# Kernel optimization log

Hardware: AMD Instinct MI355X
Metric: run time of the kernel (lower is better)

The kernel has to match this reference:

```python
import jax, jax.numpy as jnp
import numpy as np

L, H, NH, HD, F, B, S = 32, 1024, 16, 64, 2048, 2, 2048
HPH = H // NH  # hidden per attention head (hyena column split)
EPS = 1e-6
BLOCK = {0:'HCS',4:'HCS',7:'HCS',11:'HCS',14:'HCS',18:'HCS',21:'HCS',25:'HCS',28:'HCS',
         1:'HCM',5:'HCM',8:'HCM',12:'HCM',15:'HCM',19:'HCM',22:'HCM',26:'HCM',29:'HCM',
         2:'HCL',6:'HCL',9:'HCL',13:'HCL',16:'HCL',20:'HCL',23:'HCL',27:'HCL',30:'HCL',
         3:'ATT',10:'ATT',17:'ATT',24:'ATT',31:'ATT'}

def rmsnorm(x, w):
    return x * jax.lax.rsqrt(jnp.mean(x * x, -1, keepdims=True) + EPS) * w

def step_fir(u, state, w, b, flip=False, gated=False):
    # u:[B,C]  state:[B,C,cache]  w:[C,Lf]  b:[C]  (single-token FIR step)
    cache = state.shape[-1]
    w = w[:, ::-1][:, -(cache + 1):] if flip else w[:, :cache + 1]
    y = w[:, -1] * u + jnp.sum(state * w[:, :-1], -1)
    y = y + (b * u if gated else b)
    return y

def split3(z):
    # column_split_hyena=True path of _interleave_split
    r = z.reshape(z.shape[0], NH, 3 * HPH)
    x2 = r[:, :, :HPH].reshape(z.shape[0], H)
    x1 = r[:, :, HPH:2 * HPH].reshape(z.shape[0], H)
    v = r[:, :, 2 * HPH:].reshape(z.shape[0], H)
    return x2, x1, v

def mlp(x, W1, W2):
    return jax.nn.gelu(x @ W1.T) @ W2.T

def fir_block(x, n1, n2, pW, pb, oW, ob, W1, W2, sfw, sfb, h, D, fstate, istate, flip, gated):
    xn = rmsnorm(x, n1)
    z = xn @ pW.T + pb                 # [B,1,3H]
    u = z[:, -1]                       # [B,3H]
    zp = step_fir(u, fstate, sfw, sfb)
    x2, x1, v = split3(zp)
    y = step_fir(x1 * v, istate, h, D, flip=flip, gated=gated)
    y = (y * x2)[:, None]              # [B,1,H]
    x = y @ oW.T + ob + x
    return mlp(rmsnorm(x, n2), W1, W2) + x

def hcl_block(x, n1, n2, pW, pb, oW, ob, W1, W2, sfw, sfb, log_poles, residues, D, fstate, iir):
    xn = rmsnorm(x, n1)
    z = xn @ pW.T + pb
    u = z[:, -1]
    zp = step_fir(u, fstate, sfw, sfb)
    x2, x1, v = split3(zp)
    x1v = x1 * v
    iir_new = jnp.exp(log_poles) * iir + x1v[..., None]   # [B,H,SS] single-step IIR update
    res = jnp.sum(residues * iir_new, -1)
    y = (x2 * (res + D * x1v))[:, None]
    x = y @ oW.T + ob + x
    return mlp(rmsnorm(x, n2), W1, W2) + x

def att_block(x, n1, n2, qW, qb, oW, ob, W1, W2, kc, vc, cos, sin, pos):
    xn = rmsnorm(x, n1)
    qkv = (xn @ qW.T + qb).reshape(B, 1, 3, NH, HD)
    q, k, v = qkv[:, :, 0], qkv[:, :, 1], qkv[:, :, 2]
    c = jnp.concatenate([cos[pos], cos[pos]])  # [HD]
    s = jnp.concatenate([sin[pos], sin[pos]])
    rot = lambda t: jnp.concatenate([-t[..., HD // 2:], t[..., :HD // 2]], -1)
    q = q * c + rot(q) * s
    k = k * c + rot(k) * s
    kc = kc.at[:, pos].set(k[:, 0])  # KV-cache scatter write at current position
    vc = vc.at[:, pos].set(v[:, 0])
    scores = jnp.einsum('bohd,bshd->bhos', q, kc) * (HD ** -0.5)
    scores = jnp.where(jnp.arange(S) > pos, -10000.0, scores)
    aw = jax.nn.softmax(scores, -1)
    ctx = jnp.einsum('bhos,bshd->bohd', aw, vc).reshape(B, 1, H)
    x = ctx @ oW.T + ob + x
    return mlp(rmsnorm(x, n2), W1, W2) + x

def forward(x, position, norm1_w, norm2_w, proj_W, proj_b, out_W, out_b, mlp_W1, mlp_W2,
            sf_w, sf_b, hcs_h, hcs_D, hcm_h, hcm_D, hcl_logpoles, hcl_residues, hcl_D,
            fir_state, hcs_state, hcm_state, iir_state, k_cache, v_cache, rope_cos, rope_sin):
    att = 0
    for i in range(L):  # loop over 32 structurally distinct layers (static)
        t = BLOCK[i]
        cm = (norm1_w[i], norm2_w[i], proj_W[i], proj_b[i], out_W[i], out_b[i], mlp_W1[i], mlp_W2[i])
        if t == 'HCS':
            x = fir_block(x, *cm, sf_w[i], sf_b[i], hcs_h[i], hcs_D[i], fir_state[i], hcs_state[i], False, False)
        elif t == 'HCM':
            x = fir_block(x, *cm, sf_w[i], sf_b[i], hcm_h[i], hcm_D[i], fir_state[i], hcm_state[i], True, True)
        elif t == 'HCL':
            x = hcl_block(x, *cm, sf_w[i], sf_b[i], hcl_logpoles[i], hcl_residues[i], hcl_D[i], fir_state[i], iir_state[i])
        else:
            x = att_block(x, *cm, k_cache[att], v_cache[att], rope_cos, rope_sin, position)
            att += 1
    return x

def setup_inputs():
    key = jax.random.key(0)
    ks = jax.random.split(key, 24)
    g = lambda k, shape, sc: jax.random.normal(k, shape, jnp.float32) * sc
    inv_freq = 1.0 / (10000.0 ** (np.arange(0, HD, 2, dtype=np.float32) / HD))
    ang = np.arange(S, dtype=np.float32)[:, None] * inv_freq[None, :]
    return {
        'x': g(ks[0], (B, 1, H), 1.0),
        'position': 1024,
        'norm1_w': jnp.ones((L, H), jnp.float32),
        'norm2_w': jnp.ones((L, H), jnp.float32),
        'proj_W': g(ks[1], (L, 3 * H, H), H ** -0.5),
        'proj_b': jnp.zeros((L, 3 * H), jnp.float32),
        'out_W': g(ks[2], (L, H, H), 0.2 * H ** -0.5),
        'out_b': jnp.zeros((L, H), jnp.float32),
        'mlp_W1': g(ks[3], (L, F, H), H ** -0.5),
        'mlp_W2': g(ks[4], (L, H, F), 0.2 * F ** -0.5),
        'sf_w': g(ks[5], (L, 3 * H, 3), 0.4),
        'sf_b': g(ks[6], (L, 3 * H), 0.02),
        'hcs_h': g(ks[7], (L, H, 7), 0.2),
        'hcs_D': g(ks[8], (L, H), 0.2),
        'hcm_h': g(ks[9], (L, H, 128), 0.04),
        'hcm_D': g(ks[10], (L, H), 0.2),
        'hcl_logpoles': -jax.random.uniform(ks[11], (L, H, 16), jnp.float32, 0.01, 2.0),
        'hcl_residues': g(ks[12], (L, H, 16), 0.1),
        'hcl_D': g(ks[13], (L, H), 0.2),
        'fir_state': g(ks[14], (L, B, 3 * H, 2), 0.5),
        'hcs_state': g(ks[15], (L, B, H, 6), 0.5),
        'hcm_state': g(ks[16], (L, B, H, 127), 0.5),
        'iir_state': g(ks[17], (L, B, H, 16), 0.5),
        'k_cache': g(ks[18], (5, B, S, NH, HD), 1.0),
        'v_cache': g(ks[19], (5, B, S, NH, HD), 1.0),
        'rope_cos': jnp.asarray(np.cos(ang)),
        'rope_sin': jnp.asarray(np.sin(ang)),
    }

def reference(x, position, norm1_w, norm2_w, proj_W, proj_b, out_W, out_b, mlp_W1, mlp_W2,
              sf_w, sf_b, hcs_h, hcs_D, hcm_h, hcm_D, hcl_logpoles, hcl_residues, hcl_D,
              fir_state, hcs_state, hcm_state, iir_state, k_cache, v_cache, rope_cos, rope_sin):
    return forward(x, position, norm1_w, norm2_w, proj_W, proj_b, out_W, out_b, mlp_W1, mlp_W2,
                   sf_w, sf_b, hcs_h, hcs_D, hcm_h, hcm_D, hcl_logpoles, hcl_residues, hcl_D,
                   fir_state, hcs_state, hcm_state, iir_state, k_cache, v_cache, rope_cos, rope_sin)
```

## Files before the change

### kernel.cpp

```cpp
#include <hip/hip_runtime.h>
#include <hip/hip_bf16.h>
#include <math.h>

#define LAYERS 32
#define H      1024
#define H3     3072
#define NHEADS 16
#define HDIM   64
#define FF     2048
#define BATCH  2
#define SEQ    2048
#define EPSF   1e-6f

__device__ __forceinline__ float wredSum(float v) {
#pragma unroll
  for (int m = 32; m >= 1; m >>= 1) v += __shfl_xor(v, m, 64);
  return v;
}
__device__ __forceinline__ float wredMax(float v) {
#pragma unroll
  for (int m = 32; m >= 1; m >>= 1) v = fmaxf(v, __shfl_xor(v, m, 64));
  return v;
}
__device__ __forceinline__ float gelu_t(float x) {
  return 0.5f * x * (1.0f + tanhf(0.7978845608028654f * (x + 0.044715f * x * x * x)));
}
__device__ __forceinline__ float dot4(float4 a, float4 b) {
  return a.x * b.x + a.y * b.y + a.z * b.z + a.w * b.w;
}

__global__ __launch_bounds__(256) void prep_kernel(
    const float* __restrict__ sf_w, const float* __restrict__ sf_b,
    const float* __restrict__ fir_state,
    const float* __restrict__ hcs_h, const float* __restrict__ hcs_D, const float* __restrict__ hcs_state,
    const float* __restrict__ hcm_h, const float* __restrict__ hcm_D, const float* __restrict__ hcm_state,
    const float* __restrict__ lp, const float* __restrict__ resd, const float* __restrict__ hcl_D,
    const float* __restrict__ iir,
    unsigned long long kbits,
    float* __restrict__ sfd, float* __restrict__ sfc,
    float* __restrict__ mix0, float* __restrict__ mix1)
{
  int blk = blockIdx.x, tid = threadIdx.x;
  if (blk < 768) {
    int idx = blk * 256 + tid;
    int i = idx / (BATCH * H3);
    int r = idx % (BATCH * H3);
    int b = r / H3, ch = r % H3;
    const float* fs = fir_state + ((size_t)(i * BATCH + b) * H3 + ch) * 2;
    const float* sw = sf_w + ((size_t)i * H3 + ch) * 3;
    sfd[idx] = fs[0] * sw[0] + fs[1] * sw[1] + sf_b[i * H3 + ch];
    if (b == 0) sfc[i * H3 + ch] = sw[2];
  } else if (blk < 1024) {
    int idx = (blk - 768) * 256 + tid;
    int i = idx >> 11;
    int r = idx & 2047;
    int b = r >> 10, c = r & 1023;
    int kind = (int)((kbits >> (2 * i)) & 3ull);
    if (kind == 0) {
      const float* st = hcs_state + ((size_t)(i * BATCH + b) * H + c) * 6;
      const float* hh = hcs_h + ((size_t)i * H + c) * 7;
      float acc = 0.f;
#pragma unroll
      for (int k = 0; k < 6; k++) acc += st[k] * hh[k];
      mix0[idx] = acc + hcs_D[i * H + c];
      if (b == 0) mix1[i * H + c] = hh[6];
    } else if (kind == 2) {
      const float* ii = iir + ((size_t)(i * BATCH + b) * H + c) * 16;
      const float* lpp = lp + ((size_t)i * H + c) * 16;
      const float* rs = resd + ((size_t)i * H + c) * 16;
      float acc = 0.f, rsum = 0.f;
#pragma unroll
      for (int k = 0; k < 16; k++) { float rv = rs[k]; acc += rv * expf(lpp[k]) * ii[k]; rsum += rv; }
      mix0[idx] = acc;
      if (b == 0) mix1[i * H + c] = rsum + hcl_D[i * H + c];
    }
  } else {
    int w = tid >> 6, lane = tid & 63;
    int widx = (blk - 1024) * 4 + w;
    if (widx < 9 * BATCH * H) {
      int li = widx >> 11;
      int r = widx & 2047;
      int b = r >> 10, c = r & 1023;
      int i = (li >> 1) * 7 + ((li & 1) ? 5 : 1);
      const float* st = hcm_state + ((size_t)(i * BATCH + b) * H + c) * 127;
      const float* hh = hcm_h + ((size_t)i * H + c) * 128;
      float acc = 0.f;
      int k = lane;
      if (k < 127) acc += st[k] * hh[127 - k];
      k = lane + 64;
      if (k < 127) acc += st[k] * hh[127 - k];
      acc = wredSum(acc);
      if (lane == 0) {
        mix0[(i * BATCH + b) * H + c] = acc;
        if (b == 0) mix1[i * H + c] = hh[0] + hcm_D[i * H + c];
      }
    }
  }
}

template<int ROWS, bool GELU, bool HASBIAS>
__global__ __launch_bounds__(256) void gemv_norm(
    const float* __restrict__ x, const float* __restrict__ nw,
    const float* __restrict__ W, const float* __restrict__ bias,
    float* __restrict__ out)
{
  __shared__ alignas(16) float xe[BATCH * H];
  __shared__ float red[8];
  int tid = threadIdx.x, lane = tid & 63, w = tid >> 6;

  float4 xv0 = ((const float4*)x)[tid];
  float4 xv1 = ((const float4*)x)[tid + 256];
  float4 nv  = ((const float4*)nw)[tid];
  int r = blockIdx.x * 4 + w;
  const float4* rowp = (const float4*)(W + (size_t)r * H);
  float4 wv0 = rowp[lane], wv1 = rowp[lane + 64],
         wv2 = rowp[lane + 128], wv3 = rowp[lane + 192];

  float ss0 = dot4(xv0, xv0), ss1 = dot4(xv1, xv1);
  ((float4*)xe)[tid]       = make_float4(xv0.x * nv.x, xv0.y * nv.y, xv0.z * nv.z, xv0.w * nv.w);
  ((float4*)xe)[tid + 256] = make_float4(xv1.x * nv.x, xv1.y * nv.y, xv1.z * nv.z, xv1.w * nv.w);
  ss0 = wredSum(ss0); ss1 = wredSum(ss1);
  if (lane == 0) { red[w] = ss0; red[4 + w] = ss1; }
  __syncthreads();
  float s0 = rsqrtf((red[0] + red[1] + red[2] + red[3]) * (1.0f / H) + EPSF);
  float s1 = rsqrtf((red[4] + red[5] + red[6] + red[7]) * (1.0f / H) + EPSF);

  const float4* x4 = (const float4*)xe;
  float a0 = dot4(wv0, x4[lane])       + dot4(wv1, x4[lane + 64])
           + dot4(wv2, x4[lane + 128]) + dot4(wv3, x4[lane + 192]);
  float a1 = dot4(wv0, x4[lane + 256]) + dot4(wv1, x4[lane + 320])
           + dot4(wv2, x4[lane + 384]) + dot4(wv3, x4[lane + 448]);
  a0 = wredSum(a0); a1 = wredSum(a1);
  if (lane == 0) {
    float b0 = HASBIAS ? bias[r] : 0.f;
    float v0 = a0 * s0 + b0, v1 = a1 * s1 + b0;
    if (GELU) { v0 = gelu_t(v0); v1 = gelu_t(v1); }
    out[r] = v0;
    out[ROWS + r] = v1;
  }
}

__global__ __launch_bounds__(256) void mix_out_kernel(
    int kind,
    const float* __restrict__ z, const float* __restrict__ sfdL, const float* __restrict__ sfcL,
    const float* __restrict__ mix0L, const float* __restrict__ mix1L,
    const float* __restrict__ attP,
    const float* __restrict__ oW, const float* __restrict__ ob,
    const float* __restrict__ x_in, float* __restrict__ x_out)
{
  __shared__ alignas(16) float ys[BATCH * H];
  int tid = threadIdx.x, lane = tid & 63, w = tid >> 6;
  int r = blockIdx.x * 4 + w;

  if (kind < 3) {
    float x2v[8], x1v[8], vvv[8];
#pragma unroll
    for (int it = 0; it < 8; it++) {
      int e = tid + it * 256;
      int b = e >> 10, c = e & 1023;
      int n = c >> 6, d = c & 63;
      int base = n * 192 + d;
      x2v[it] = sfcL[base] * z[b * H3 + base] + sfdL[b * H3 + base];
      x1v[it] = sfcL[base + 64] * z[b * H3 + base + 64] + sfdL[b * H3 + base + 64];
      vvv[it] = sfcL[base + 128] * z[b * H3 + base + 128] + sfdL[b * H3 + base + 128];
    }
    const float4* rowp = (const float4*)(oW + (size_t)r * H);
    float4 wv0 = rowp[lane], wv1 = rowp[lane + 64],
           wv2 = rowp[lane + 128], wv3 = rowp[lane + 192];
#pragma unroll
    for (int it = 0; it < 8; it++) {
      int e = tid + it * 256;
      int b = e >> 10, c = e & 1023;
      float t = x1v[it] * vvv[it];
      ys[e] = (mix1L[c] * t + mix0L[b * H + c]) * x2v[it];
    }
    __syncthreads();
    const float4* y4 = (const float4*)ys;
    float a0 = dot4(wv0, y4[lane])       + dot4(wv1, y4[lane + 64])
             + dot4(wv2, y4[lane + 128]) + dot4(wv3, y4[lane + 192]);
    float a1 = dot4(wv0, y4[lane + 256]) + dot4(wv1, y4[lane + 320])
             + dot4(wv2, y4[lane + 384]) + dot4(wv3, y4[lane + 448]);
    a0 = wredSum(a0); a1 = wredSum(a1);
    if (lane == 0) {
      x_out[r]     = a0 + ob[r] + x_in[r];
      x_out[H + r] = a1 + ob[r] + x_in[H + r];
    }
  } else {
    const float4* rowp = (const float4*)(oW + (size_t)r * H);
    float4 wv0 = rowp[lane], wv1 = rowp[lane + 64],
           wv2 = rowp[lane + 128], wv3 = rowp[lane + 192];
#pragma unroll
    for (int it = 0; it < 8; it++) {
      int e = tid + it * 256;
      int b = e >> 10, c = e & 1023;
      int n = c >> 6, d = c & 63;
      float M = -1e30f;
#pragma unroll
      for (int sp = 0; sp < 8; sp++) M = fmaxf(M, attP[((sp * BATCH + b) * NHEADS + n) * 66 + 64]);
      float Ls = 0.f, num = 0.f;
#pragma unroll
      for (int sp = 0; sp < 8; sp++) {
        const float* P = attP + ((sp * BATCH + b) * NHEADS + n) * 66;
        float wgt = expf(P[64] - M);
        Ls += wgt * P[65];
        num += wgt * P[d];
      }
      ys[e] = num / Ls;
    }
    __syncthreads();
    const float4* y4 = (const float4*)ys;
    float a0 = dot4(wv0, y4[lane])       + dot4(wv1, y4[lane + 64])
             + dot4(wv2, y4[lane + 128]) + dot4(wv3, y4[lane + 192]);
    float a1 = dot4(wv0, y4[lane + 256]) + dot4(wv1, y4[lane + 320])
             + dot4(wv2, y4[lane + 384]) + dot4(wv3, y4[lane + 448]);
    a0 = wredSum(a0); a1 = wredSum(a1);
    if (lane == 0) {
      x_out[r]     = a0 + ob[r] + x_in[r];
      x_out[H + r] = a1 + ob[r] + x_in[H + r];
    }
  }
}

__global__ __launch_bounds__(256) void gemv_mlp2(
    const float* __restrict__ h, const float* __restrict__ W2,
    const float* __restrict__ xM, float* __restrict__ x_out)
{
  __shared__ alignas(16) float hs[BATCH * FF];
  int tid = threadIdx.x, lane = tid & 63, w = tid >> 6;
  float4 h0 = ((const float4*)h)[tid];
  float4 h1 = ((const float4*)h)[tid + 256];
  float4 h2 = ((const float4*)h)[tid + 512];
  float4 h3 = ((const float4*)h)[tid + 768];
  int r = blockIdx.x * 4 + w;
  const float4* rowp = (const float4*)(W2 + (size_t)r * FF);
  float4 wv[8];
#pragma unroll
  for (int j = 0; j < 8; j++) wv[j] = rowp[lane + 64 * j];

  ((float4*)hs)[tid]       = h0;
  ((float4*)hs)[tid + 256] = h1;
  ((float4*)hs)[tid + 512] = h2;
  ((float4*)hs)[tid + 768] = h3;
  __syncthreads();

  const float4* h4 = (const float4*)hs;
  float a0 = 0.f, a1 = 0.f;
#pragma unroll
  for (int j = 0; j < 8; j++) {
    a0 += dot4(wv[j], h4[lane + 64 * j]);
    a1 += dot4(wv[j], h4[lane + 64 * j + 512]);
  }
  a0 = wredSum(a0); a1 = wredSum(a1);
  if (lane == 0) {
    x_out[r]     = a0 + xM[r];
    x_out[H + r] = a1 + xM[H + r];
  }
}

__global__ __launch_bounds__(256) void attn_kernel(
    const float* __restrict__ z, const int* __restrict__ posp,
    const float* __restrict__ kc, const float* __restrict__ vc,
    const float* __restrict__ cosT, const float* __restrict__ sinT,
    float* __restrict__ P)
{
  int sp = blockIdx.x & 7, n = (blockIdx.x >> 3) & 15, b = blockIdx.x >> 7;
  int pos = *posp;
  __shared__ alignas(16) float q_s[HDIM], k_s[HDIM], v_s[HDIM];
  __shared__ float eg[256];
  __shared__ float redA[4];
  __shared__ alignas(16) float osum[4][HDIM];
  int tid = threadIdx.x, lane = tid & 63, w = tid >> 6;

  if (tid < 64) {
    int d = tid, j = d & 31;
    float cs = cosT[pos * 32 + j], sn = sinT[pos * 32 + j];
    float qv = z[b * H3 + n * 64 + d];
    float qo = z[b * H3 + n * 64 + ((d + 32) & 63)];
    q_s[d] = ((d < 32) ? (qv * cs - qo * sn) : (qv * cs + qo * sn)) * 0.125f;
    float kv = z[b * H3 + 1024 + n * 64 + d];
    float ko = z[b * H3 + 1024 + n * 64 + ((d + 32) & 63)];
    k_s[d] = (d < 32) ? (kv * cs - ko * sn) : (kv * cs + ko * sn);
    v_s[d] = z[b * H3 + 2048 + n * 64 + d];
  }
  __syncthreads();

  int s = sp * 256 + tid;
  float logit = -1e30f;
  if (s <= pos) {
    const float4* k4 = (s == pos) ? (const float4*)k_s
                                  : (const float4*)(kc + (((size_t)b * SEQ + s) * NHEADS + n) * HDIM);
    const float4* q4 = (const float4*)q_s;
    float acc = 0.f;
#pragma unroll
    for (int j = 0; j < 16; j++) acc += dot4(k4[j], q4[j]);
    logit = acc;
  }
  float m = wredMax(logit);
  if (lane == 0) redA[w] = m;
  __syncthreads();
  m = fmaxf(fmaxf(redA[0], redA[1]), fmaxf(redA[2], redA[3]));
  float e = (s <= pos) ? expf(logit - m) : 0.f;
  eg[tid] = e;
  float ps = wredSum(e);
  __syncthreads();
  if (lane == 0) redA[w] = ps;
  __syncthreads();
  float lsum = redA[0] + redA[1] + redA[2] + redA[3];

  int dgrp = lane & 15, srow = lane >> 4;
  float4 acc = make_float4(0.f, 0.f, 0.f, 0.f);
#pragma unroll 4
  for (int it = 0; it < 16; it++) {
    int sl = w * 64 + it * 4;
    if (sp * 256 + sl > pos) break;
    int sli = sl + srow;
    int ss = sp * 256 + sli;
    float ev = eg[sli];
    const float4* v4 = (ss == pos) ? (const float4*)v_s
                                   : (const float4*)(vc + (((size_t)b * SEQ + ss) * NHEADS + n) * HDIM);
    float4 vv = v4[dgrp];
    acc.x += ev * vv.x; acc.y += ev * vv.y; acc.z += ev * vv.z; acc.w += ev * vv.w;
  }
#pragma unroll
  for (int mm = 16; mm <= 32; mm <<= 1) {
    acc.x += __shfl_xor(acc.x, mm, 64);
    acc.y += __shfl_xor(acc.y, mm, 64);
    acc.z += __shfl_xor(acc.z, mm, 64);
    acc.w += __shfl_xor(acc.w, mm, 64);
  }
  if (srow == 0) ((float4*)osum[w])[dgrp] = acc;
  __syncthreads();
  float* Pp = P + ((size_t)(sp * BATCH + b) * NHEADS + n) * 66;
  if (tid < 64) Pp[tid] = osum[0][tid] + osum[1][tid] + osum[2][tid] + osum[3][tid];
  if (tid == 64) Pp[64] = m;
  if (tid == 65) Pp[65] = lsum;
}

extern "C" void kernel_launch(void* const* d_in, const int* in_sizes, int n_in,
                              void* d_out, int out_size, void* d_ws, size_t ws_size,
                              hipStream_t stream) {
  (void)in_sizes; (void)n_in; (void)out_size; (void)ws_size;
  const float* x0    = (const float*)d_in[0];
  const int*   posp  = (const int*)d_in[1];
  const float* n1    = (const float*)d_in[2];
  const float* n2    = (const float*)d_in[3];
  const float* pW    = (const float*)d_in[4];
  const float* pb    = (const float*)d_in[5];
  const float* oW    = (const float*)d_in[6];
  const float* ob    = (const float*)d_in[7];
  const float* W1    = (const float*)d_in[8];
  const float* W2    = (const float*)d_in[9];
  const float* sfw   = (const float*)d_in[10];
  const float* sfb   = (const float*)d_in[11];
  const float* hcs_h = (const float*)d_in[12];
  const float* hcs_D = (const float*)d_in[13];
  const float* hcm_h = (const float*)d_in[14];
  const float* hcm_D = (const float*)d_in[15];
  const float* lp    = (const float*)d_in[16];
  const float* resd  = (const float*)d_in[17];
  const float* hclD  = (const float*)d_in[18];
  const float* fir   = (const float*)d_in[19];
  const float* hcsS  = (const float*)d_in[20];
  const float* hcmS  = (const float*)d_in[21];
  const float* iir   = (const float*)d_in[22];
  const float* kc    = (const float*)d_in[23];
  const float* vc    = (const float*)d_in[24];
  const float* cosT  = (const float*)d_in[25];
  const float* sinT  = (const float*)d_in[26];

  float* ws    = (float*)d_ws;
  float* xbuf0 = ws;
  float* xbuf1 = ws + 2048;
  float* xM    = ws + 4096;
  float* zbuf  = ws + 6144;
  float* hbuf  = ws + 12288;
  float* attP  = ws + 16384;
  float* sfd   = ws + 33280;
  float* sfc   = ws + 229888;
  float* mix0  = ws + 328192;
  float* mix1  = ws + 393728;

  static const int KIND[LAYERS] = {0,1,2,3,0,1,2,0,1,2,3,0,1,2,0,1,2,3,0,1,2,0,1,2,3,0,1,2,0,1,2,3};
  unsigned long long kbits = 0ull;
  for (int i = 0; i < LAYERS; i++) kbits |= ((unsigned long long)KIND[i]) << (2 * i);

  prep_kernel<<<5632, 256, 0, stream>>>(sfw, sfb, fir, hcs_h, hcs_D, hcsS,
      hcm_h, hcm_D, hcmS, lp, resd, hclD, iir, kbits, sfd, sfc, mix0, mix1);

  const float* xsrc = x0;
  int att = 0;
  for (int i = 0; i < LAYERS; i++) {
    gemv_norm<H3, false, true><<<H3 / 4, 256, 0, stream>>>(
        xsrc, n1 + i * H, pW + (size_t)i * H3 * H, pb + i * H3, zbuf);
    if (KIND[i] == 3) {
      attn_kernel<<<256, 256, 0, stream>>>(
          zbuf, posp, kc + (size_t)att * BATCH * SEQ * NHEADS * HDIM,
          vc + (size_t)att * BATCH * SEQ * NHEADS * HDIM, cosT, sinT, attP);
      att++;
    }
    mix_out_kernel<<<H / 4, 256, 0, stream>>>(
        KIND[i], zbuf, sfd + (size_t)i * BATCH * H3, sfc + (size_t)i * H3,
        mix0 + (size_t)i * BATCH * H, mix1 + (size_t)i * H, attP,
        oW + (size_t)i * H * H, ob + i * H, xsrc, xM);
    gemv_norm<FF, true, false><<<FF / 4, 256, 0, stream>>>(
        xM, n2 + i * H, W1 + (size_t)i * FF * H, nullptr, hbuf);
    float* xout = (i == LAYERS - 1) ? (float*)d_out : ((i & 1) ? xbuf1 : xbuf0);
    gemv_mlp2<<<H / 4, 256, 0, stream>>>(
        hbuf, W2 + (size_t)i * H * FF, xM, xout);
    xsrc = xout;
  }
}
```

Measured before the change: 681.1 us.

## Prefetch next layer's weights into cache via extra blocks in current kernels

Adds extra thread blocks to the prep, mix_out, MLP-up and MLP-down kernels. These blocks only stream the next layer's pW, oW, W1 and W2 matrices in 32KB chunks, so the data is pulled into the shared cache hierarchy ahead of use. The aim is to overlap next-layer weight fetch with the small, latency-bound GEMV kernels of the current layer, so later kernels hit cache instead of HBM. The cost is that the prefetch blocks compete with the real work for bandwidth and CUs. Their benefit depends on the data staying resident in the last-level cache until it is consumed.

Result: slower. 757.9 us (+11.3%).

```diff
diff --git a/kernel.cpp b/kernel.cpp
--- a/kernel.cpp
+++ b/kernel.cpp
@@ -29,6 +29,17 @@
   return a.x * b.x + a.y * b.y + a.z * b.z + a.w * b.w;
 }
 
+__device__ __forceinline__ void pf32(const float4* __restrict__ p, int chunk) {
+  const float4* b = p + (size_t)chunk * 2048 + threadIdx.x;
+  float a0 = 0.f, a1 = 0.f, a2 = 0.f, a3 = 0.f;
+#pragma unroll
+  for (int k = 0; k < 8; k++) {
+    float4 v = b[k * 256];
+    a0 += v.x; a1 += v.y; a2 += v.z; a3 += v.w;
+  }
+  asm volatile("" :: "v"(a0), "v"(a1), "v"(a2), "v"(a3));
+}
+
 __global__ __launch_bounds__(256) void prep_kernel(
     const float* __restrict__ sf_w, const float* __restrict__ sf_b,
     const float* __restrict__ fir_state,
@@ -38,9 +49,19 @@
     const float* __restrict__ iir,
     unsigned long long kbits,
     float* __restrict__ sfd, float* __restrict__ sfc,
-    float* __restrict__ mix0, float* __restrict__ mix1)
+    float* __restrict__ mix0, float* __restrict__ mix1,
+    const float4* __restrict__ pW0, const float4* __restrict__ oW0,
+    const float4* __restrict__ W10, const float4* __restrict__ W20)
 {
   int blk = blockIdx.x, tid = threadIdx.x;
+  if (blk >= 5632) {
+    int idx = blk - 5632;
+    if (idx < 384) pf32(pW0, idx);
+    else if (idx < 512) pf32(oW0, idx - 384);
+    else if (idx < 768) pf32(W10, idx - 512);
+    else pf32(W20, idx - 768);
+    return;
+  }
   if (blk < 768) {
     int idx = blk * 256 + tid;
     int i = idx / (BATCH * H3);
@@ -102,11 +123,22 @@
 __global__ __launch_bounds__(256) void gemv_norm(
     const float* __restrict__ x, const float* __restrict__ nw,
     const float* __restrict__ W, const float* __restrict__ bias,
-    float* __restrict__ out)
+    float* __restrict__ out,
+    const float4* __restrict__ f0, int c0,
+    const float4* __restrict__ f1, int c1,
+    const float4* __restrict__ f2, int c2)
 {
   __shared__ alignas(16) float xe[BATCH * H];
   __shared__ float red[8];
   int tid = threadIdx.x, lane = tid & 63, w = tid >> 6;
+  const int NFUNC = ROWS / 4;
+  if (blockIdx.x >= NFUNC) {
+    int idx = blockIdx.x - NFUNC;
+    if (idx < c0) pf32(f0, idx);
+    else if (idx < c0 + c1) pf32(f1, idx - c0);
+    else if (idx < c0 + c1 + c2) pf32(f2, idx - c0 - c1);
+    return;
+  }
 
   float4 xv0 = ((const float4*)x)[tid];
   float4 xv1 = ((const float4*)x)[tid + 256];
@@ -146,10 +178,16 @@
     const float* __restrict__ mix0L, const float* __restrict__ mix1L,
     const float* __restrict__ attP,
     const float* __restrict__ oW, const float* __restrict__ ob,
-    const float* __restrict__ x_in, float* __restrict__ x_out)
+    const float* __restrict__ x_in, float* __restrict__ x_out,
+    const float4* __restrict__ f0, int c0)
 {
   __shared__ alignas(16) float ys[BATCH * H];
   int tid = threadIdx.x, lane = tid & 63, w = tid >> 6;
+  if (blockIdx.x >= 256) {
+    int idx = blockIdx.x - 256;
+    if (idx < c0) pf32(f0, idx);
+    return;
+  }
   int r = blockIdx.x * 4 + w;
 
   if (kind < 3) {
@@ -223,10 +261,18 @@
 
 __global__ __launch_bounds__(256) void gemv_mlp2(
     const float* __restrict__ h, const float* __restrict__ W2,
-    const float* __restrict__ xM, float* __restrict__ x_out)
+    const float* __restrict__ xM, float* __restrict__ x_out,
+    const float4* __restrict__ f0, int c0,
+    const float4* __restrict__ f1, int c1)
 {
   __shared__ alignas(16) float hs[BATCH * FF];
   int tid = threadIdx.x, lane = tid & 63, w = tid >> 6;
+  if (blockIdx.x >= 256) {
+    int idx = blockIdx.x - 256;
+    if (idx < c0) pf32(f0, idx);
+    else if (idx < c0 + c1) pf32(f1, idx - c0);
+    return;
+  }
   float4 h0 = ((const float4*)h)[tid];
   float4 h1 = ((const float4*)h)[tid + 256];
   float4 h2 = ((const float4*)h)[tid + 512];
@@ -384,29 +430,47 @@
   unsigned long long kbits = 0ull;
   for (int i = 0; i < LAYERS; i++) kbits |= ((unsigned long long)KIND[i]) << (2 * i);
 
-  prep_kernel<<<5632, 256, 0, stream>>>(sfw, sfb, fir, hcs_h, hcs_D, hcsS,
-      hcm_h, hcm_D, hcmS, lp, resd, hclD, iir, kbits, sfd, sfc, mix0, mix1);
+  prep_kernel<<<5632 + 1024, 256, 0, stream>>>(sfw, sfb, fir, hcs_h, hcs_D, hcsS,
+      hcm_h, hcm_D, hcmS, lp, resd, hclD, iir, kbits, sfd, sfc, mix0, mix1,
+      (const float4*)pW, (const float4*)oW, (const float4*)W1, (const float4*)W2);
 
   const float* xsrc = x0;
   int att = 0;
   for (int i = 0; i < LAYERS; i++) {
+    int nx = i + 1;
+    bool hasNext = (nx < LAYERS);
+    const float4* pWn  = hasNext ? (const float4*)(pW + (size_t)nx * H3 * H) : (const float4*)pW;
+    const float4* oWn  = hasNext ? (const float4*)(oW + (size_t)nx * H * H) : (const float4*)oW;
+    const float4* W1n  = hasNext ? (const float4*)(W1 + (size_t)nx * FF * H) : (const float4*)W1;
+    const float4* W2n  = hasNext ? (const float4*)(W2 + (size_t)nx * H * FF) : (const float4*)W2;
+    int cm = hasNext ? 352 : 0;
+    int cw1a = hasNext ? 32 : 0;
+    int cw1b = hasNext ? 128 : 0;
+    int cw1c = hasNext ? 192 : 0;
+    int cw2a = hasNext ? 64 : 0;
+    int cw2b = hasNext ? 256 : 0;
+
     gemv_norm<H3, false, true><<<H3 / 4, 256, 0, stream>>>(
-        xsrc, n1 + i * H, pW + (size_t)i * H3 * H, pb + i * H3, zbuf);
+        xsrc, n1 + i * H, pW + (size_t)i * H3 * H, pb + i * H3, zbuf,
+        (const float4*)pW, 0, (const float4*)pW, 0, (const float4*)pW, 0);
     if (KIND[i] == 3) {
       attn_kernel<<<256, 256, 0, stream>>>(
           zbuf, posp, kc + (size_t)att * BATCH * SEQ * NHEADS * HDIM,
           vc + (size_t)att * BATCH * SEQ * NHEADS * HDIM, cosT, sinT, attP);
       att++;
     }
-    mix_out_kernel<<<H / 4, 256, 0, stream>>>(
+    mix_out_kernel<<<256 + cm, 256, 0, stream>>>(
         KIND[i], zbuf, sfd + (size_t)i * BATCH * H3, sfc + (size_t)i * H3,
         mix0 + (size_t)i * BATCH * H, mix1 + (size_t)i * H, attP,
-        oW + (size_t)i * H * H, ob + i * H, xsrc, xM);
-    gemv_norm<FF, true, false><<<FF / 4, 256, 0, stream>>>(
-        xM, n2 + i * H, W1 + (size_t)i * FF * H, nullptr, hbuf);
+        oW + (size_t)i * H * H, ob + i * H, xsrc, xM,
+        pWn, cm);
+    gemv_norm<FF, true, false><<<FF / 4 + cw1a + cw1b + cw1c, 256, 0, stream>>>(
+        xM, n2 + i * H, W1 + (size_t)i * FF * H, nullptr, hbuf,
+        pWn + (size_t)352 * 2048, cw1a, oWn, cw1b, W1n, cw1c);
     float* xout = (i == LAYERS - 1) ? (float*)d_out : ((i & 1) ? xbuf1 : xbuf0);
-    gemv_mlp2<<<H / 4, 256, 0, stream>>>(
-        hbuf, W2 + (size_t)i * H * FF, xM, xout);
+    gemv_mlp2<<<256 + cw2a + cw2b, 256, 0, stream>>>(
+        hbuf, W2 + (size_t)i * H * FF, xM, xout,
+        W1n + (size_t)192 * 2048, cw2a, W2n, cw2b);
     xsrc = xout;
   }
 }
```
